# Performance work log

Measured on AMD Instinct MI355X. Metric: run time of the kernel, lower is better.

## Reference

```python
import jax, jax.numpy as jnp
import numpy as np

N_NODES = 30522
HID = 768
N_EDGES = 488352
B, S = 4, 512
L = 12  # transformer_layers
C = 100  # num classes in pos-neg codebook graph


def setup_inputs() -> dict:
    key = jax.random.key(0)
    ks = jax.random.split(key, 20)
    inp = {}
    inp["word_embs"] = jax.random.normal(ks[0], (N_NODES, HID), dtype=jnp.float32)
    inp["input_ids"] = jax.random.randint(ks[1], (B, S), 0, N_NODES + 1)  # N_NODES = padding row
    inp["class_ids"] = jax.random.randint(ks[2], (B, S), 0, C + 1)
    inp["mask"] = jax.random.randint(ks[3], (B, S, 1), 0, 2).astype(bool)
    inp["co_edge_index"] = jax.random.randint(ks[4], (2, N_EDGES), 0, N_NODES)
    inp["co_edge_weight"] = jax.random.uniform(ks[5], (N_EDGES,), dtype=jnp.float32)
    inp["re_edge_index"] = jax.random.randint(ks[6], (2, N_EDGES), 0, N_NODES)
    inp["re_edge_weight"] = jax.random.uniform(ks[7], (N_EDGES,), dtype=jnp.float32)
    pn_graph = jax.random.uniform(ks[8], (C + 1, N_NODES), dtype=jnp.float32) * 0.01
    inp["pn_graph"] = pn_graph.at[-1].set(0.0)  # padding row of zeros
    sc = 0.02
    inp["co_W"] = jax.random.normal(ks[9], (3, HID, HID), dtype=jnp.float32) * sc
    inp["co_b"] = jnp.zeros((3, HID), jnp.float32)
    inp["re_W"] = jax.random.normal(ks[10], (3, HID, HID), dtype=jnp.float32) * sc
    inp["re_b"] = jnp.zeros((3, HID), jnp.float32)
    inp["pn_W"] = jax.random.normal(ks[11], (HID, HID), dtype=jnp.float32) * sc  # [out,in] 1x1 conv
    inp["pn_b"] = jnp.zeros((HID,), jnp.float32)
    # zero_convs are zero-initialized in the original; use small random so math is non-trivial
    inp["zero_w"] = jax.random.normal(ks[12], (L, HID, HID), dtype=jnp.float32) * sc
    inp["zero_b"] = jnp.zeros((L, HID), jnp.float32)
    inp["zero_w_pos"] = jax.random.normal(ks[13], (L, HID, HID), dtype=jnp.float32) * sc
    inp["zero_b_pos"] = jnp.zeros((L, HID), jnp.float32)
    return inp


def _gcn_layer(x, src, dst, ew, W, b, n):
    # PyG GCNConv: add self-loops (weight 1), symmetric normalization
    deg = jax.ops.segment_sum(ew, dst, num_segments=n) + 1.0
    dinv = jnp.where(deg > 0, jax.lax.rsqrt(deg), 0.0)
    norm = dinv[src] * ew * dinv[dst]  # [E]
    h = x @ W  # [n, H]
    agg = jax.ops.segment_sum(norm[:, None] * h[src], dst, num_segments=n)
    agg = agg + h * (dinv * dinv)[:, None]  # self-loop contribution
    return agg + b


def _gcn_stack(x, edge_index, ew, Ws, bs, ids):
    src, dst = edge_index[0], edge_index[1]
    n = x.shape[0]
    h = x
    acc = None
    for i in range(3):
        h = jax.nn.relu(_gcn_layer(h, src, dst, ew, Ws[i], bs[i], n))
        pad = jnp.concatenate([h, jnp.zeros((1, h.shape[-1]), h.dtype)], axis=0)
        g = pad[ids]  # [B, S, H] gather with padding row
        acc = g if acc is None else acc + g
    return acc / 3.0


def _zero_conv_layers(tok, w, b):
    # 1x1 conv over hidden channels for each of L layers: [B,S,H] x [L,O,H] -> [L,B,S,O]
    return jnp.einsum("bsh,loh->lbso", tok, w) + b[:, None, None, :]


def reference(word_embs, input_ids, class_ids, mask,
              co_edge_index, co_edge_weight, re_edge_index, re_edge_weight,
              pn_graph, co_W, co_b, re_W, re_b, pn_W, pn_b,
              zero_w, zero_b, zero_w_pos, zero_b_pos):
    Bq, Sq = input_ids.shape
    H = word_embs.shape[-1]
    Lq = zero_w.shape[0]
    inv_mask = (~mask).astype(word_embs.dtype)  # [B,S,1]
    zero_pad = jnp.zeros((Lq, Bq, 1, H), word_embs.dtype)

    co = _gcn_stack(word_embs, co_edge_index, co_edge_weight, co_W, co_b, input_ids)  # [B,S,H]
    re = _gcn_stack(word_embs, re_edge_index, re_edge_weight, re_W, re_b, input_ids)

    # NOTE: original uses self.zero_convs (not a separate set) for BOTH co and re
    co_l = _zero_conv_layers(co, zero_w, zero_b) * inv_mask[None]
    re_l = _zero_conv_layers(re, zero_w, zero_b) * inv_mask[None]
    co_l = jnp.concatenate([zero_pad, co_l], axis=2)  # [L,B,S+1,H]
    re_l = jnp.concatenate([zero_pad, re_l], axis=2)

    # PosNegCodebook: 1x1 conv on codebook, then dense-graph matmul, gathered by class
    cb = word_embs @ pn_W.T + pn_b  # [N, H]
    pn = (pn_graph @ cb)[class_ids]  # [B,S,H] (same math as graph[class_ids] @ cb)
    pn_l = _zero_conv_layers(pn, zero_w_pos, zero_b_pos)
    pn_l = jnp.concatenate([zero_pad, pn_l], axis=2)

    return (co_l, re_l, pn_l)
```

## Files before the change

### kernel.cpp

```cpp
#include <hip/hip_runtime.h>
#include <stdint.h>

typedef unsigned int u32;
typedef unsigned short u16;
typedef __attribute__((ext_vector_type(8))) short short8;
typedef __attribute__((ext_vector_type(4))) float f32x4;

#define N_NODESC 30522
#define HIDC 768
#define NEC 488352
#define TOKM 2048
#define LLAY 12
#define NCLS 101
#define M_PAD 30720
#define ZNC (LLAY*HIDC)
#define OUT_SET (LLAY*4*513*HIDC)
#define PN_KCHUNK 512
#define NBLK 120
#define NN1 (N_NODESC+1)
#define G8_LDS 131072

__device__ __forceinline__ float bl(u32 u){ return __uint_as_float(u<<16); }
__device__ __forceinline__ float bh(u32 u){ return __uint_as_float(u & 0xffff0000u); }
__device__ __forceinline__ u32 f2b1(float f){ u32 x=__float_as_uint(f); return (x + 0x7fffu + ((x>>16)&1u))>>16; }
__device__ __forceinline__ u32 pack2(float a, float b){ return f2b1(a) | (f2b1(b)<<16); }

__device__ __forceinline__ void mfma16(f32x4& d, short8 a, short8 b){
  asm volatile("v_mfma_f32_16x16x32_bf16 %0, %1, %2, %0" : "+v"(d) : "v"(a), "v"(b));
}
__device__ __forceinline__ void async16(const void* g, void* l){
  __builtin_amdgcn_global_load_lds((const __attribute__((address_space(1))) u32*)g,
                                   (__attribute__((address_space(3))) u32*)l, 16, 0, 0);
}

__global__ void k_invmask(const void* __restrict__ mask, float* __restrict__ invm){
  __shared__ int s_byte, s_flt;
  int t = threadIdx.x;
  const unsigned char* mb = (const unsigned char*)mask;
  const u32* mw = (const u32*)mask;
  int lb=0, lf=0;
  for(int i=t;i<2048;i+=256) if((i&3)!=0 && mb[i]!=0) lb=1;
  for(int i=t;i<512;i+=256) if(mw[i]==0x3F800000u) lf=1;
  if(t==0){ s_byte=0; s_flt=0; }
  __syncthreads();
  if(lb) s_byte=1;
  if(lf) s_flt=1;
  __syncthreads();
  int mode = s_flt ? 2 : (s_byte ? 1 : 0);
  for(int p=t;p<2048;p+=256){
    int mv = (mode==1) ? (int)mb[p] : (int)(mw[p]!=0u);
    invm[p] = mv ? 0.f : 1.f;
  }
}

__global__ void k_needed(const int* __restrict__ ids, u32* __restrict__ needed){
  int p = blockIdx.x*256 + threadIdx.x;
  if(p < TOKM){ int id = ids[p]; if(id < N_NODESC) needed[id] = 1u; }
}

__global__ void k_conv(const float* __restrict__ src, u16* __restrict__ dst, int ndw){
  int i = blockIdx.x*256 + threadIdx.x;
  if(i < ndw) ((u32*)dst)[i] = pack2(src[2*i], src[2*i+1]);
}
__global__ void k_conv_pad(const float* __restrict__ src, u16* __restrict__ dst, int srcRows, int padRows){
  int i = blockIdx.x*256 + threadIdx.x;
  if(i >= padRows*384) return;
  int row = i/384; int c2 = (i - row*384)*2;
  float lo=0.f, hi=0.f;
  if(row < srcRows){ const float* s = src + (size_t)row*HIDC + c2; lo=s[0]; hi=s[1]; }
  ((u32*)dst)[i] = pack2(lo, hi);
}
__global__ void k_pnb(const float* __restrict__ png, u16* __restrict__ pnb){
  int i = blockIdx.x*256 + threadIdx.x;
  if(i >= 128*(M_PAD/2)) return;
  int row = i/(M_PAD/2); int k2 = (i - row*(M_PAD/2))*2;
  float lo=0.f, hi=0.f;
  if(row < NCLS){
    const float* s = png + (size_t)row*N_NODESC;
    if(k2 < N_NODESC) lo = s[k2];
    if(k2+1 < N_NODESC) hi = s[k2+1];
  }
  ((u32*)pnb)[i] = pack2(lo, hi);
}
__global__ void k_transposeW2(const float* __restrict__ coW, const float* __restrict__ reW,
                              u16* __restrict__ Wt2){
  int g = blockIdx.y;
  int i = blockIdx.x*256 + threadIdx.x;
  if(i >= 3*HIDC*384) return;
  const float* W = g ? reW : coW;
  int mat = i/(HIDC*384); int rem = i - mat*HIDC*384;
  int n = rem/384; int kd = rem - n*384;
  const float* Wm = W + (size_t)mat*HIDC*HIDC;
  float lo = Wm[(size_t)(2*kd)*HIDC + n];
  float hi = Wm[(size_t)(2*kd+1)*HIDC + n];
  ((u32*)Wt2)[(size_t)g*3*HIDC*384 + (size_t)mat*HIDC*384 + (size_t)n*384 + kd] = pack2(lo, hi);
}

__global__ void k_degcnt2(const int* __restrict__ coei, const int* __restrict__ reei,
                          const float* __restrict__ coew, const float* __restrict__ reew,
                          float* __restrict__ deg2, int* __restrict__ cnt2){
  int g = blockIdx.y;
  const int* ei = g ? reei : coei;
  const float* ew = g ? reew : coew;
  int e = blockIdx.x*256 + threadIdx.x;
  if(e < NEC){ int d = ei[NEC+e]; atomicAdd(&deg2[(size_t)g*N_NODESC + d], ew[e]); atomicAdd(&cnt2[(size_t)g*N_NODESC + d], 1); }
}
__global__ void k_dinv2(const float* __restrict__ deg2, float* __restrict__ dinvA, float* __restrict__ dinvB){
  int g = blockIdx.y;
  int v = blockIdx.x*256 + threadIdx.x;
  if(v < N_NODESC){
    float d = deg2[(size_t)g*N_NODESC + v] + 1.f;
    dinvA[(size_t)g*N_NODESC + v] = rsqrtf(d);
    dinvB[(size_t)g*N_NODESC + v] = 1.f/d;
  }
}
__global__ void k_scan1(const int* __restrict__ cnt2, int* __restrict__ part2){
  __shared__ int wt[4];
  int g = blockIdx.y, b = blockIdx.x, t = threadIdx.x;
  int lane = t & 63, w = t >> 6;
  int i = b*256 + t;
  int v = (i < N_NODESC) ? cnt2[(size_t)g*N_NODESC + i] : 0;
  int x = v;
  #pragma unroll
  for(int off=1; off<64; off<<=1){ int y = __shfl_up(x, off); if(lane>=off) x += y; }
  if(lane==63) wt[w] = x;
  __syncthreads();
  if(t==0) part2[g*NBLK + b] = wt[0]+wt[1]+wt[2]+wt[3];
}
__global__ void k_scan2(int* __restrict__ part2, int* __restrict__ rp2){
  __shared__ int w0tot;
  int g = blockIdx.x, t = threadIdx.x;
  int lane = t & 63, w = t >> 6;
  int v = (t < NBLK) ? part2[g*NBLK + t] : 0;
  int x = v;
  #pragma unroll
  for(int off=1; off<64; off<<=1){ int y = __shfl_up(x, off); if(lane>=off) x += y; }
  if(w==0 && lane==63) w0tot = x;
  __syncthreads();
  int incl = x + (w ? w0tot : 0);
  int excl = incl - v;
  if(t < NBLK) part2[g*NBLK + t] = excl;
  if(t == 127) rp2[(size_t)g*NN1 + N_NODESC] = incl;
}
__global__ void k_scan3(const int* __restrict__ cnt2, const int* __restrict__ part2,
                        int* __restrict__ rp2, int* __restrict__ cur2){
  __shared__ int wt[4];
  int g = blockIdx.y, b = blockIdx.x, t = threadIdx.x;
  int lane = t & 63, w = t >> 6;
  int i = b*256 + t;
  int v = (i < N_NODESC) ? cnt2[(size_t)g*N_NODESC + i] : 0;
  int x = v;
  #pragma unroll
  for(int off=1; off<64; off<<=1){ int y = __shfl_up(x, off); if(lane>=off) x += y; }
  if(lane==63) wt[w] = x;
  __syncthreads();
  int wpre = 0;
  #pragma unroll
  for(int j=0;j<4;j++) if(j<w) wpre += wt[j];
  int excl = x - v + wpre + part2[g*NBLK + b];
  if(i < N_NODESC){ rp2[(size_t)g*NN1 + i] = excl; cur2[(size_t)g*N_NODESC + i] = excl; }
}
__global__ void k_scatter2(const int* __restrict__ coei, const int* __restrict__ reei,
                           const float* __restrict__ coew, const float* __restrict__ reew,
                           const float* __restrict__ dinvA, int* __restrict__ cur2,
                           float2* __restrict__ emeta){
  int g = blockIdx.y;
  const int* ei = g ? reei : coei;
  const float* ew = g ? reew : coew;
  int e = blockIdx.x*256 + threadIdx.x;
  if(e < NEC){
    int s = ei[e], d = ei[NEC+e];
    int pos = atomicAdd(&cur2[(size_t)g*N_NODESC + d], 1);
    float nrm = dinvA[(size_t)g*N_NODESC + s]*ew[e]*dinvA[(size_t)g*N_NODESC + d];
    emeta[(size_t)g*NEC + pos] = make_float2(__int_as_float(s), nrm);
  }
}

__global__ __launch_bounds__(256)
void k_spmm(const u16* __restrict__ hW, const int* __restrict__ rp,
            const float2* __restrict__ emeta, const float* __restrict__ dinv2,
            const float* __restrict__ bias, u16* __restrict__ hout,
            const u32* __restrict__ needed){
  int v = blockIdx.x*4 + (threadIdx.x>>6);
  if(v >= N_NODESC) return;
  if(needed && !needed[v]) return;
  int lane = threadIdx.x & 63;
  const u32* H = (const u32*)hW;
  float acc[12];
  #pragma unroll
  for(int q=0;q<12;q++) acc[q]=0.f;
  int e0 = rp[v], e1 = rp[v+1];
  int e = e0;
  for(; e+4<=e1; e+=4){
    float2 m0=emeta[e], m1=emeta[e+1], m2=emeta[e+2], m3=emeta[e+3];
    const u32* r0 = H + (size_t)__float_as_int(m0.x)*384 + lane;
    const u32* r1 = H + (size_t)__float_as_int(m1.x)*384 + lane;
    const u32* r2 = H + (size_t)__float_as_int(m2.x)*384 + lane;
    const u32* r3 = H + (size_t)__float_as_int(m3.x)*384 + lane;
    u32 u0[6],u1[6],u2[6],u3[6];
    #pragma unroll
    for(int q=0;q<6;q++){ u0[q]=r0[q*64]; u1[q]=r1[q*64]; u2[q]=r2[q*64]; u3[q]=r3[q*64]; }
    #pragma unroll
    for(int q=0;q<6;q++){
      acc[2*q]   += m0.y*bl(u0[q]) + m1.y*bl(u1[q]) + m2.y*bl(u2[q]) + m3.y*bl(u3[q]);
      acc[2*q+1] += m0.y*bh(u0[q]) + m1.y*bh(u1[q]) + m2.y*bh(u2[q]) + m3.y*bh(u3[q]);
    }
  }
  for(; e<e1; ++e){
    float2 mm = emeta[e];
    const u32* r = H + (size_t)__float_as_int(mm.x)*384 + lane;
    #pragma unroll
    for(int q=0;q<6;q++){ u32 u = r[q*64]; acc[2*q] += mm.y*bl(u); acc[2*q+1] += mm.y*bh(u); }
  }
  { float wgt = dinv2[v];
    const u32* r = H + (size_t)v*384 + lane;
    #pragma unroll
    for(int q=0;q<6;q++){ u32 u = r[q*64]; acc[2*q] += wgt*bl(u); acc[2*q+1] += wgt*bh(u); }
  }
  const float2* B2 = (const float2*)bias;
  u32* O = (u32*)hout + (size_t)v*384 + lane;
  #pragma unroll
  for(int q=0;q<6;q++){
    float2 bb = B2[lane + 64*q];
    float x0 = fmaxf(acc[2*q]+bb.x, 0.f);
    float x1 = fmaxf(acc[2*q+1]+bb.y, 0.f);
    O[q*64] = pack2(x0, x1);
  }
}

__global__ void k_gather(const u16* __restrict__ h, const int* __restrict__ ids,
                         float2* __restrict__ tokf, u16* __restrict__ tokb, int phase){
  int d = blockIdx.x*256 + threadIdx.x;
  if(d >= TOKM*384) return;
  int p = d/384, q = d - p*384;
  int id = ids[p];
  float x0=0.f, x1=0.f;
  if(id < N_NODESC){ u32 u = ((const u32*)h)[(size_t)id*384 + q]; x0 = bl(u)*(1.f/3.f); x1 = bh(u)*(1.f/3.f); }
  float2 cur;
  if(phase==0){ cur.x=x0; cur.y=x1; }
  else { cur = tokf[d]; cur.x += x0; cur.y += x1; }
  if(phase==2) ((u32*)tokb)[d] = pack2(cur.x, cur.y);
  else tokf[d] = cur;
}

__global__ void k_gather_pn(const float* __restrict__ GT, const int* __restrict__ cids, u16* __restrict__ tokb){
  int d = blockIdx.x*256 + threadIdx.x;
  if(d >= TOKM*384) return;
  int p = d/384, q = d - p*384;
  int cid = cids[p];
  float lo = GT[(size_t)(2*q)*128 + cid];
  float hi = GT[(size_t)(2*q+1)*128 + cid];
  ((u32*)tokb)[d] = pack2(lo, hi);
}

__global__ void k_zerocol(float* __restrict__ out){
  int i = blockIdx.x*256 + threadIdx.x;
  if(i >= 3*LLAY*4*HIDC) return;
  int set = i/(LLAY*4*HIDC); int rem = i - set*(LLAY*4*HIDC);
  int l = rem/(4*HIDC); int rem2 = rem - l*(4*HIDC);
  int b = rem2/HIDC; int o = rem2 - b*HIDC;
  out[(size_t)set*OUT_SET + (size_t)(l*4+b)*513*HIDC + o] = 0.f;
}

#define G8_AOFF(b) ((b)*65536)
#define G8_BOFF(b) ((b)*65536 + 32768)

__device__ __forceinline__ void g8_stage(const u16* __restrict__ src, int ldk, int g0, int kt,
                                         char* half_base, int tid){
  const int lane = tid & 63;
  const int csw = ((lane&7) ^ (lane>>3)) << 3;
  const u16* s0 = src + (size_t)(g0 + (tid>>3))*ldk + (kt + csw);
  const u16* s1 = src + (size_t)(g0 + 64 + (tid>>3))*ldk + (kt + csw);
  async16(s0, half_base + (size_t)tid*16);
  async16(s1, half_base + 8192 + (size_t)tid*16);
}

__device__ __forceinline__ void g8_core(const u16* __restrict__ A, const u16* __restrict__ Bt,
                                        int K, int m0, int n0,
                                        f32x4 (&acc)[8][4], char* LDS, int tid){
  const int lane = tid & 63;
  const int wid = tid >> 6;
  const int wr = wid >> 2, wc = wid & 3;
  const int NK = K >> 6;

  g8_stage(Bt, K, n0,      0, LDS + G8_BOFF(0),         tid);
  g8_stage(Bt, K, n0+128,  0, LDS + G8_BOFF(0) + 16384, tid);
  g8_stage(A,  K, m0,      0, LDS + G8_AOFF(0),         tid);
  g8_stage(A,  K, m0+128,  0, LDS + G8_AOFF(0) + 16384, tid);
  g8_stage(Bt, K, n0,     64, LDS + G8_BOFF(1),         tid);
  g8_stage(Bt, K, n0+128, 64, LDS + G8_BOFF(1) + 16384, tid);
  asm volatile("s_waitcnt vmcnt(4)" ::: "memory");
  __builtin_amdgcn_sched_barrier(0);
  __builtin_amdgcn_s_barrier();
  __builtin_amdgcn_sched_barrier(0);

  short8 bf8[8];
  for(int T=0; T<NK; ++T){
    const int buf = T & 1;
    const char* Ab = LDS + G8_AOFF(buf) + wr*16384;
    const char* Bb = LDS + G8_BOFF(buf) + (wc>>1)*16384;
    #pragma unroll
    for(int q=0; q<4; ++q){
      if(q==0){
        #pragma unroll
        for(int n=0;n<4;n++){
          #pragma unroll
          for(int kk=0;kk<2;kk++){
            int row = ((wc&1)<<6) + (n<<4) + (lane&15);
            int cb = ((kk<<6) + ((lane>>4)<<4)) ^ ((lane&7)<<4);
            bf8[n*2+kk] = *(const short8*)(Bb + row*128 + cb);
          }
        }
      }
      short8 af[2][2];
      #pragma unroll
      for(int j=0;j<2;j++){
        #pragma unroll
        for(int kk=0;kk<2;kk++){
          int row = ((2*q+j)<<4) + (lane&15);
          int cb = ((kk<<6) + ((lane>>4)<<4)) ^ ((lane&7)<<4);
          af[j][kk] = *(const short8*)(Ab + row*128 + cb);
        }
      }
      if(q==0 && T+1<NK) g8_stage(A,  K, m0,      (T+1)<<6, LDS + G8_AOFF((T+1)&1),         tid);
      if(q==1 && T+1<NK) g8_stage(A,  K, m0+128,  (T+1)<<6, LDS + G8_AOFF((T+1)&1) + 16384, tid);
      if(q==2 && T+2<NK) g8_stage(Bt, K, n0,      (T+2)<<6, LDS + G8_BOFF(buf),             tid);
      if(q==3 && T+2<NK) g8_stage(Bt, K, n0+128,  (T+2)<<6, LDS + G8_BOFF(buf) + 16384,     tid);
      if(q==3){
        if(T <= NK-3)      asm volatile("s_waitcnt vmcnt(4)" ::: "memory");
        else if(T == NK-2) asm volatile("s_waitcnt vmcnt(0)" ::: "memory");
      }
      __builtin_amdgcn_sched_barrier(0);
      __builtin_amdgcn_s_barrier();
      __builtin_amdgcn_sched_barrier(0);
      __builtin_amdgcn_s_setprio(1);
      #pragma unroll
      for(int j=0;j<2;j++){
        #pragma unroll
        for(int n=0;n<4;n++){
          #pragma unroll
          for(int kk=0;kk<2;kk++) mfma16(acc[2*q+j][n], af[j][kk], bf8[n*2+kk]);
        }
      }
      __builtin_amdgcn_s_setprio(0);
      __builtin_amdgcn_sched_barrier(0);
      __builtin_amdgcn_s_barrier();
      __builtin_amdgcn_sched_barrier(0);
    }
  }
}

__device__ __forceinline__ void g8_split(int ntM, int ntN, int& bm, int& bn){
  int nwg = ntM*ntN;
  int bid = (int)blockIdx.x;
  int wg = (bid & 7)*(nwg>>3) + (bid>>3);
  if(ntN <= ntM){ bm = wg/ntN; bn = wg - bm*ntN; }
  else          { bn = wg/ntM; bm = wg - bn*ntM; }
}

template<int MODE>
__global__ __launch_bounds__(512,2)
void gemm8p_bf16(const u16* __restrict__ A, const u16* __restrict__ Bt,
                 int M, int N, int K,
                 u16* __restrict__ outB, const float* __restrict__ bias){
  extern __shared__ char LDS[];
  const int tid = threadIdx.x;
  const int lane = tid & 63;
  const int wid = tid >> 6;
  const int wr = wid >> 2, wc = wid & 3;
  int bm, bn;
  g8_split(M>>8, N>>8, bm, bn);
  const int m0 = bm << 8, n0 = bn << 8;

  f32x4 acc[8][4];
  f32x4 zv = {0.f,0.f,0.f,0.f};
  #pragma unroll
  for(int m=0;m<8;m++){
    #pragma unroll
    for(int n=0;n<4;n++) acc[m][n] = zv;
  }
  g8_core(A, Bt, K, m0, n0, acc, LDS, tid);

  const int rbase = (lane>>4)<<2;
  const int cbase = lane & 15;
  #pragma unroll
  for(int m=0;m<8;m++){
    int row0 = m0 + (wr<<7) + (m<<4) + rbase;
    #pragma unroll
    for(int n=0;n<4;n++){
      int col = n0 + (wc<<6) + (n<<4) + cbase;
      #pragma unroll
      for(int r=0;r<4;r++){
        float v = acc[m][n][r];
        if(MODE==2) v += bias[row0+r];
        outB[(size_t)(row0+r)*N + col] = (u16)f2b1(v);
      }
    }
  }
}

__global__ __launch_bounds__(512,2)
void gemm8p_zc(const u16* __restrict__ TOKALL, const u16* __restrict__ ZWALL,
               const float* __restrict__ zb, const float* __restrict__ zbp,
               const float* __restrict__ invm, float* __restrict__ out){
  extern __shared__ char LDS[];
  const int set = blockIdx.z;
  const u16* A  = TOKALL + (size_t)set*TOKM*HIDC;
  const u16* Bt = ZWALL + (set==2 ? (size_t)ZNC*HIDC : 0);
  const float* bias = (set==2) ? zbp : zb;
  const bool use_mask = (set != 2);
  float* o = out + (size_t)set*OUT_SET;

  const int tid = threadIdx.x;
  const int lane = tid & 63;
  const int wid = tid >> 6;
  const int wr = wid >> 2, wc = wid & 3;
  int bm, bn;
  g8_split(TOKM>>8, ZNC>>8, bm, bn);
  const int m0 = bm << 8, n0 = bn << 8;

  f32x4 acc[8][4];
  f32x4 zv = {0.f,0.f,0.f,0.f};
  #pragma unroll
  for(int m=0;m<8;m++){
    #pragma unroll
    for(int n=0;n<4;n++) acc[m][n] = zv;
  }
  g8_core(A, Bt, HIDC, m0, n0, acc, LDS, tid);

  const int l = n0 / HIDC;
  const int oc0 = n0 - l*HIDC;
  const int lo = lane & 15, hi = lane >> 4;

  #pragma unroll
  for(int pass=0; pass<2; ++pass){
    __syncthreads();
    if(wr == pass){
      #pragma unroll
      for(int m=0;m<8;m++){
        #pragma unroll
        for(int n=0;n<4;n++){
          int col = (wc<<6) + (n<<4) + lo;
          float badd = bias[n0 + col];
          #pragma unroll
          for(int r=0;r<4;r++){
            int lr = (m<<4) + (hi<<2) + r;
            *(float*)(LDS + (size_t)lr*1024 + ((col<<2) ^ ((lr&7)<<4))) = acc[m][n][r] + badd;
          }
        }
      }
    }
    __syncthreads();
    #pragma unroll
    for(int i=0;i<16;i++){
      int lr = (i<<3) + wid;
      int rr = m0 + (pass<<7) + lr;
      int b = rr >> 9, s = rr & 511;
      f32x4 v = *(const f32x4*)(LDS + (size_t)lr*1024 + ((lane<<4) ^ ((lr&7)<<4)));
      if(use_mask){ float w = invm[rr]; v = v * w; }
      *(f32x4*)(o + (size_t)((l*4+b)*513 + (s+1))*HIDC + oc0 + (lane<<2)) = v;
    }
  }
}

__global__ __launch_bounds__(256,2)
void gemm_splitk(const u16* __restrict__ A, const u16* __restrict__ Bt,
                 int M, int N, int K, float* __restrict__ outF, int kchunk){
  __shared__ u16 As[128*64];
  __shared__ u16 Bs[128*64];
  const int t = threadIdx.x;
  const int lane = t & 63;
  const int w = t >> 6;
  const int wr = w >> 1, wc = w & 1;
  int nchunks = (K + kchunk - 1)/kchunk;
  int bm = (int)blockIdx.x / nchunks;
  int ch = (int)blockIdx.x - bm*nchunks;
  int k0 = ch*kchunk, k1 = k0 + kchunk; if(k1 > K) k1 = K;
  const int m0 = bm << 7, n0 = 0;

  f32x4 zv = {0.f,0.f,0.f,0.f};
  f32x4 acc[4][4];
  #pragma unroll
  for(int m=0;m<4;m++){
    #pragma unroll
    for(int n=0;n<4;n++) acc[m][n] = zv;
  }
  const int srow = t >> 3;
  const int scol = (t & 7) << 3;
  const u16* Ag = A + (size_t)(m0 + srow)*K + scol;
  const u16* Bg = Bt + (size_t)(n0 + srow)*K + scol;
  u16* Al = &As[t*8];
  u16* Bl = &Bs[t*8];

  for(int kt=k0; kt<k1; kt+=64){
    __syncthreads();
    #pragma unroll
    for(int i=0;i<4;i++){
      async16(Ag + (size_t)(i*32)*K + kt, Al + i*2048);
      async16(Bg + (size_t)(i*32)*K + kt, Bl + i*2048);
    }
    __syncthreads();
    #pragma unroll
    for(int kk=0; kk<64; kk+=32){
      const int ko = kk + ((lane>>4)<<3);
      short8 af[4], bfv[4];
      #pragma unroll
      for(int m=0;m<4;m++) af[m] = *(const short8*)&As[((wr<<6)+(m<<4)+(lane&15))*64 + ko];
      #pragma unroll
      for(int n=0;n<4;n++) bfv[n] = *(const short8*)&Bs[((wc<<6)+(n<<4)+(lane&15))*64 + ko];
      #pragma unroll
      for(int m=0;m<4;m++){
        #pragma unroll
        for(int n=0;n<4;n++) mfma16(acc[m][n], af[m], bfv[n]);
      }
    }
  }
  const int rbase = (lane>>4)<<2;
  const int cbase = lane & 15;
  #pragma unroll
  for(int m=0;m<4;m++){
    int row0 = m0 + (wr<<6) + (m<<4) + rbase;
    #pragma unroll
    for(int n=0;n<4;n++){
      int col = n0 + (wc<<6) + (n<<4) + cbase;
      #pragma unroll
      for(int r=0;r<4;r++) atomicAdd(&outF[(size_t)(row0+r)*N + col], acc[m][n][r]);
    }
  }
}

extern "C" void kernel_launch(void* const* d_in, const int* in_sizes, int n_in,
                              void* d_out, int out_size, void* d_ws, size_t ws_size,
                              hipStream_t stream){
  const float* word  = (const float*)d_in[0];
  const int*   ids   = (const int*)d_in[1];
  const int*   cids  = (const int*)d_in[2];
  const void*  mask  = d_in[3];
  const int*   co_ei = (const int*)d_in[4];
  const float* co_ew = (const float*)d_in[5];
  const int*   re_ei = (const int*)d_in[6];
  const float* re_ew = (const float*)d_in[7];
  const float* png   = (const float*)d_in[8];
  const float* co_W  = (const float*)d_in[9];
  const float* co_b  = (const float*)d_in[10];
  const float* re_W  = (const float*)d_in[11];
  const float* re_b  = (const float*)d_in[12];
  const float* pn_W  = (const float*)d_in[13];
  const float* pn_b  = (const float*)d_in[14];
  const float* zw    = (const float*)d_in[15];
  const float* zb    = (const float*)d_in[16];
  const float* zwp   = (const float*)d_in[17];
  const float* zbp   = (const float*)d_in[18];
  float* out = (float*)d_out;

  hipFuncSetAttribute((const void*)gemm8p_bf16<0>, hipFuncAttributeMaxDynamicSharedMemorySize, G8_LDS);
  hipFuncSetAttribute((const void*)gemm8p_bf16<2>, hipFuncAttributeMaxDynamicSharedMemorySize, G8_LDS);
  hipFuncSetAttribute((const void*)gemm8p_zc,      hipFuncAttributeMaxDynamicSharedMemorySize, G8_LDS);

  char* wsb = (char*)d_ws;
  size_t off = 0;
  auto alloc = [&](size_t bytes)->void*{ void* p = wsb + off; off += (bytes + 255) & ~(size_t)255; return p; };
  u16* WORDB = (u16*)alloc((size_t)M_PAD*HIDC*2);
  u16* BUFB  = (u16*)alloc((size_t)M_PAD*HIDC*2);
  u16* BUFX  = (u16*)alloc((size_t)M_PAD*HIDC*2);
  u16* ZWALL = (u16*)alloc((size_t)2*ZNC*HIDC*2);
  u16* WT2   = (u16*)alloc((size_t)2*3*HIDC*HIDC*2);
  u16* PNWB  = (u16*)alloc((size_t)HIDC*HIDC*2);
  u16* PNB   = (u16*)alloc((size_t)128*M_PAD*2);
  u16* TOKALL= (u16*)alloc((size_t)3*TOKM*HIDC*2);
  float2* TOKF = (float2*)alloc((size_t)TOKM*HIDC*4);
  float* GT   = (float*)alloc((size_t)HIDC*128*4);
  float* DEG2 = (float*)alloc((size_t)2*N_NODESC*4);
  int*   CNT2 = (int*)alloc((size_t)2*N_NODESC*4);
  float* DINVA = (float*)alloc((size_t)2*N_NODESC*4);
  float* DINVB = (float*)alloc((size_t)2*N_NODESC*4);
  int*   RP2  = (int*)alloc((size_t)2*NN1*4);
  int*   CUR2 = (int*)alloc((size_t)2*N_NODESC*4);
  int*   PART2= (int*)alloc((size_t)2*NBLK*4);
  float2* EMETA=(float2*)alloc((size_t)2*NEC*8);
  u32*   NEED = (u32*)alloc((size_t)N_NODESC*4);
  float* INVM = (float*)alloc((size_t)TOKM*4);
  (void)ws_size; (void)in_sizes; (void)n_in; (void)out_size;

  const int GD_TOK = (TOKM*384 + 255)/256;
  const int GD_E   = (NEC + 255)/256;
  const int SPMM_GD  = (N_NODESC + 3)/4;
  const int PN_NCHUNKS = M_PAD/PN_KCHUNK;
  const int G_PN  = (HIDC/128)*PN_NCHUNKS;
  const int G8_GCN = (M_PAD/256)*(HIDC/256);
  const int G8_CBT = (HIDC/256)*(M_PAD/256);
  const int G8_ZC  = (TOKM/256)*(ZNC/256);

  hipMemsetAsync(NEED, 0, (size_t)N_NODESC*4, stream);
  hipMemsetAsync(DEG2, 0, (size_t)2*N_NODESC*4, stream);
  hipMemsetAsync(CNT2, 0, (size_t)2*N_NODESC*4, stream);
  k_invmask<<<1,256,0,stream>>>(mask, INVM);
  k_needed<<<(TOKM+255)/256,256,0,stream>>>(ids, NEED);
  k_conv<<<(HIDC*HIDC/2 + 255)/256,256,0,stream>>>(pn_W, PNWB, HIDC*HIDC/2);
  k_conv<<<(ZNC*HIDC/2 + 255)/256,256,0,stream>>>(zw, ZWALL, ZNC*HIDC/2);
  k_conv<<<(ZNC*HIDC/2 + 255)/256,256,0,stream>>>(zwp, ZWALL + (size_t)ZNC*HIDC, ZNC*HIDC/2);
  k_conv_pad<<<(M_PAD*384 + 255)/256,256,0,stream>>>(word, WORDB, N_NODESC, M_PAD);
  k_transposeW2<<<dim3((3*HIDC*384 + 255)/256, 2),256,0,stream>>>(co_W, re_W, WT2);

  k_degcnt2<<<dim3(GD_E,2),256,0,stream>>>(co_ei, re_ei, co_ew, re_ew, DEG2, CNT2);
  k_dinv2<<<dim3((N_NODESC+255)/256,2),256,0,stream>>>(DEG2, DINVA, DINVB);
  k_scan1<<<dim3(NBLK,2),256,0,stream>>>(CNT2, PART2);
  k_scan2<<<2,128,0,stream>>>(PART2, RP2);
  k_scan3<<<dim3(NBLK,2),256,0,stream>>>(CNT2, PART2, RP2, CUR2);
  k_scatter2<<<dim3(GD_E,2),256,0,stream>>>(co_ei, re_ei, co_ew, re_ew, DINVA, CUR2, EMETA);

  gemm8p_bf16<2><<<G8_CBT,512,G8_LDS,stream>>>(PNWB, WORDB, HIDC, M_PAD, HIDC, BUFX, pn_b);
  k_pnb<<<(128*(M_PAD/2) + 255)/256,256,0,stream>>>(png, PNB);
  hipMemsetAsync(GT, 0, (size_t)HIDC*128*4, stream);
  gemm_splitk<<<G_PN,256,0,stream>>>(BUFX, PNB, HIDC, 128, M_PAD, GT, PN_KCHUNK);
  k_gather_pn<<<GD_TOK,256,0,stream>>>(GT, cids, TOKALL + (size_t)2*TOKM*HIDC);

  auto run_graph = [&](int g, const float* bf, u16* tokb){
    const int* rp = RP2 + (size_t)g*NN1;
    const float2* em = EMETA + (size_t)g*NEC;
    const float* di2 = DINVB + (size_t)g*N_NODESC;
    const u16* X = WORDB;
    for(int i=0;i<3;i++){
      gemm8p_bf16<0><<<G8_GCN,512,G8_LDS,stream>>>(X, WT2 + ((size_t)g*3 + i)*HIDC*HIDC,
                                                   M_PAD, HIDC, HIDC, BUFB, nullptr);
      k_spmm<<<SPMM_GD,256,0,stream>>>(BUFB, rp, em, di2, bf + i*HIDC, BUFX,
                                       (i==2) ? NEED : nullptr);
      k_gather<<<GD_TOK,256,0,stream>>>(BUFX, ids, TOKF, tokb, i);
      X = BUFX;
    }
  };
  run_graph(0, co_b, TOKALL);
  run_graph(1, re_b, TOKALL + (size_t)TOKM*HIDC);

  dim3 zgrid(G8_ZC, 1, 3);
  gemm8p_zc<<<zgrid,512,G8_LDS,stream>>>(TOKALL, ZWALL, zb, zbp, INVM, out);
  k_zerocol<<<(3*LLAY*4*HIDC + 255)/256,256,0,stream>>>(out);
}
```

Measured before the change: 1.286 ms.

## Split GCN SpMM into XCD-pinned column slabs for L2 locality

Adds a slab-partitioned SpMM kernel in which each block handles one 128-column slab of H for four nodes. Block IDs are mapped so each XCD (bid&7) works mostly on a single slab, with two helper XCDs sharing the remaining work, so the gathered rows of H for a given slab stay in that XCD's L2. Edge metadata is read with nontemporal loads and outputs are written with nontemporal stores to avoid polluting the cache. The first two layers use it, while the last layer keeps the old kernel because it needs the NEED mask. The cost is rereading edge metadata six times and launching a much larger grid.

Result: slower. 1.531 ms (+19.1%).

```diff
diff --git a/kernel.cpp b/kernel.cpp
--- a/kernel.cpp
+++ b/kernel.cpp
@@ -20,6 +20,12 @@
 #define NN1 (N_NODESC+1)
 #define G8_LDS 131072
 
+#define SP_NB   7631
+#define SP_MAIN 5723
+#define SP_HELP 1908
+#define SP_J    5724
+#define SP_GRID (8*SP_J)
+
 __device__ __forceinline__ float bl(u32 u){ return __uint_as_float(u<<16); }
 __device__ __forceinline__ float bh(u32 u){ return __uint_as_float(u & 0xffff0000u); }
 __device__ __forceinline__ u32 f2b1(float f){ u32 x=__float_as_uint(f); return (x + 0x7fffu + ((x>>16)&1u))>>16; }
@@ -31,6 +37,11 @@
 __device__ __forceinline__ void async16(const void* g, void* l){
   __builtin_amdgcn_global_load_lds((const __attribute__((address_space(1))) u32*)g,
                                    (__attribute__((address_space(3))) u32*)l, 16, 0, 0);
+}
+__device__ __forceinline__ void em_dec(double d, int& s, float& w){
+  unsigned long long b = __double_as_longlong(d);
+  s = (int)(u32)b;
+  w = __uint_as_float((u32)(b>>32));
 }
 
 __global__ void k_invmask(const void* __restrict__ mask, float* __restrict__ invm){
@@ -226,6 +237,59 @@
     float x1 = fmaxf(acc[2*q+1]+bb.y, 0.f);
     O[q*64] = pack2(x0, x1);
   }
+}
+
+__global__ __launch_bounds__(256)
+void k_spmm_slab(const u16* __restrict__ hW, const int* __restrict__ rp,
+                 const float2* __restrict__ emeta, const float* __restrict__ dinv2,
+                 const float* __restrict__ bias, u16* __restrict__ hout){
+  int bid = (int)blockIdx.x;
+  int xcd = bid & 7, j = bid >> 3;
+  int q, nb;
+  if(xcd < 6){
+    if(j >= SP_MAIN) return;
+    q = xcd; nb = j;
+  } else {
+    int s3 = j / SP_HELP;
+    if(s3 > 2) return;
+    q = (xcd==6) ? s3 : 3+s3;
+    nb = SP_MAIN + (j - s3*SP_HELP);
+    if(nb >= SP_NB) return;
+  }
+  int v = nb*4 + (threadIdx.x>>6);
+  if(v >= N_NODESC) return;
+  int lane = threadIdx.x & 63;
+  const u32* Hq = (const u32*)hW + q*64 + lane;
+  const double* em8 = (const double*)emeta;
+  float a0 = 0.f, a1 = 0.f;
+  int e0 = rp[v], e1 = rp[v+1];
+  int e = e0;
+  for(; e+4<=e1; e+=4){
+    int s0,s1,s2,s3; float w0,w1,w2,w3;
+    em_dec(__builtin_nontemporal_load(em8+e  ), s0, w0);
+    em_dec(__builtin_nontemporal_load(em8+e+1), s1, w1);
+    em_dec(__builtin_nontemporal_load(em8+e+2), s2, w2);
+    em_dec(__builtin_nontemporal_load(em8+e+3), s3, w3);
+    u32 u0 = Hq[(size_t)s0*384];
+    u32 u1 = Hq[(size_t)s1*384];
+    u32 u2 = Hq[(size_t)s2*384];
+    u32 u3 = Hq[(size_t)s3*384];
+    a0 += w0*bl(u0) + w1*bl(u1) + w2*bl(u2) + w3*bl(u3);
+    a1 += w0*bh(u0) + w1*bh(u1) + w2*bh(u2) + w3*bh(u3);
+  }
+  for(; e<e1; ++e){
+    int ss; float ww;
+    em_dec(__builtin_nontemporal_load(em8+e), ss, ww);
+    u32 u = Hq[(size_t)ss*384];
+    a0 += ww*bl(u); a1 += ww*bh(u);
+  }
+  { u32 u = Hq[(size_t)v*384];
+    float wgt = dinv2[v];
+    a0 += wgt*bl(u); a1 += wgt*bh(u); }
+  float2 bb = ((const float2*)bias)[q*64 + lane];
+  float x0 = fmaxf(a0+bb.x, 0.f);
+  float x1 = fmaxf(a1+bb.y, 0.f);
+  __builtin_nontemporal_store(pack2(x0,x1), (u32*)hout + (size_t)v*384 + q*64 + lane);
 }
 
 __global__ void k_gather(const u16* __restrict__ h, const int* __restrict__ ids,
@@ -623,8 +687,10 @@
     for(int i=0;i<3;i++){
       gemm8p_bf16<0><<<G8_GCN,512,G8_LDS,stream>>>(X, WT2 + ((size_t)g*3 + i)*HIDC*HIDC,
                                                    M_PAD, HIDC, HIDC, BUFB, nullptr);
-      k_spmm<<<SPMM_GD,256,0,stream>>>(BUFB, rp, em, di2, bf + i*HIDC, BUFX,
-                                       (i==2) ? NEED : nullptr);
+      if(i==2)
+        k_spmm<<<SPMM_GD,256,0,stream>>>(BUFB, rp, em, di2, bf + i*HIDC, BUFX, NEED);
+      else
+        k_spmm_slab<<<SP_GRID,256,0,stream>>>(BUFB, rp, em, di2, bf + i*HIDC, BUFX);
       k_gather<<<GD_TOK,256,0,stream>>>(BUFX, ids, TOKF, tokb, i);
       X = BUFX;
     }
```
